# Kernel optimization log

Measured on AMD Instinct MI355X. Metric: run time of the kernel, lower is better.

## Reference

```python
import jax, jax.numpy as jnp
import numpy as np

N_NODES = 50000

def _graph_conv(x, src, dst, W, b, n):
    # DGL GraphConv, norm='both': D_dst^{-1/2} * sum_edges(D_src^{-1/2} * (x W)) + b
    xw = x @ W  # [N, out]
    ones = jnp.ones(src.shape, jnp.float32)
    deg_out = jnp.maximum(jax.ops.segment_sum(ones, src, num_segments=n), 1.0)
    deg_in = jnp.maximum(jax.ops.segment_sum(ones, dst, num_segments=n), 1.0)
    norm_src = deg_out ** -0.5
    norm_dst = deg_in ** -0.5
    msg = xw[src] * norm_src[src][:, None]          # [E, out] gather
    agg = jax.ops.segment_sum(msg, dst, num_segments=n)  # [N, out] scatter-add
    return agg * norm_dst[:, None] + b


def _rgcn_layer(x, src, dst, W, b, n):
    # HeteroGraphConv with aggregate='sum' over relations
    out = _graph_conv(x, src[0], dst[0], W[0], b[0], n)
    for r in range(1, src.shape[0]):
        out = out + _graph_conv(x, src[r], dst[r], W[r], b[r], n)
    return out


def setup_inputs() -> dict:
    key = jax.random.key(0)
    ks = jax.random.split(key, 9)
    R, E = 3, 200000
    din, dhid, dout = 128, 128, 64
    x = jax.random.normal(ks[0], (N_NODES, din), jnp.float32)
    src = jax.random.randint(ks[1], (R, E), 0, N_NODES, jnp.int32)
    dst = jax.random.randint(ks[2], (R, E), 0, N_NODES, jnp.int32)
    neg_src = jax.random.randint(ks[3], (E,), 0, N_NODES, jnp.int32)
    neg_dst = jax.random.randint(ks[4], (E,), 0, N_NODES, jnp.int32)
    W1 = jax.random.normal(ks[5], (R, din, dhid), jnp.float32) / np.sqrt(din)
    b1 = jnp.zeros((R, dhid), jnp.float32)
    W2 = jax.random.normal(ks[6], (R, dhid, dout), jnp.float32) / np.sqrt(dhid)
    b2 = jnp.zeros((R, dout), jnp.float32)
    return {"x": x, "src": src, "dst": dst, "neg_src": neg_src,
            "neg_dst": neg_dst, "W1": W1, "b1": b1, "W2": W2, "b2": b2}


def reference(x, src, dst, neg_src, neg_dst, W1, b1, W2, b2):
    n = x.shape[0]
    h = jax.nn.relu(_rgcn_layer(x, src, dst, W1, b1, n))
    h = _rgcn_layer(h, src, dst, W2, b2, n)  # [N, out]
    # HeteroDotProductPredictor on etype = relation 0 (u_dot_v -> [E, 1])
    pos = jnp.sum(h[src[0]] * h[dst[0]], axis=-1, keepdims=True)
    neg = jnp.sum(h[neg_src] * h[neg_dst], axis=-1, keepdims=True)
    return pos, neg
```

## Files before the change

kernel.cpp:

```cpp
#include <hip/hip_runtime.h>

#define N_NODES 50000
#define E_EDGES 200000
#define R_REL 3
#define D_IN 128
#define D_HID 128
#define D_OUT 64
#define N_SCAN (R_REL * N_NODES)
#define BCAP 16
#define OVCAP 4096

typedef __attribute__((ext_vector_type(8))) short bf16x8;
typedef __attribute__((ext_vector_type(4))) float f32x4;

__device__ inline unsigned short f2bf(float v) {
    union { float f; unsigned int u; } x; x.f = v;
    unsigned int r = x.u + 0x7fffu + ((x.u >> 16) & 1u);
    return (unsigned short)(r >> 16);
}
__device__ inline float bf2f(unsigned short h) {
    union { unsigned int u; float f; } x; x.u = ((unsigned int)h) << 16; return x.f;
}
__device__ inline float bf_lo(unsigned int p) {
    union { unsigned int u; float f; } x; x.u = p << 16; return x.f;
}
__device__ inline float bf_hi(unsigned int p) {
    union { unsigned int u; float f; } x; x.u = p & 0xffff0000u; return x.f;
}

__global__ __launch_bounds__(256) void k_zero_i32(int* __restrict__ p, int n) {
    int i = blockIdx.x * 256 + threadIdx.x;
    if (i < n) p[i] = 0;
}

__global__ __launch_bounds__(256) void k_count_prep(const int* __restrict__ src,
                                                    const int* __restrict__ dst,
                                                    const float* __restrict__ x,
                                                    const float* __restrict__ W1,
                                                    const float* __restrict__ W2,
                                                    const float* __restrict__ b1,
                                                    int* __restrict__ deg_out,
                                                    int* __restrict__ cnt_in,
                                                    int* __restrict__ ov_cnt,
                                                    uint2* __restrict__ ovlist,
                                                    int* __restrict__ bucket,
                                                    unsigned int* __restrict__ xb,
                                                    unsigned short* __restrict__ w1t_h,
                                                    unsigned short* __restrict__ w1t_l,
                                                    unsigned short* __restrict__ w2t_h,
                                                    unsigned short* __restrict__ w2t_l,
                                                    float* __restrict__ bsum) {
    int g = blockIdx.x / 5;
    int m = blockIdx.x % 5;
    int t = threadIdx.x;
    if (m < 3) {
        int eb = g * 3 + m;
        int i = eb * 256 + t;
        if (i >= R_REL * E_EDGES) return;
        int r = i / E_EDGES;
        int s = src[i];
        int d = dst[i];
        atomicAdd(&deg_out[r * N_NODES + s], 1);
        int bin = r * N_NODES + d;
        int pos = atomicAdd(&cnt_in[bin], 1);
        if (pos < BCAP) {
            bucket[bin * BCAP + pos] = s;
        } else {
            int oi = atomicAdd(ov_cnt, 1);
            if (oi < OVCAP) {
                uint2 e;
                e.x = (unsigned int)bin;
                e.y = (unsigned int)s;
                ovlist[oi] = e;
            }
        }
    } else {
        int pb = g * 2 + (m - 3);
        int qbase = pb * 1024;
#pragma unroll
        for (int k = 0; k < 4; k++) {
            int q = qbase + k * 256 + t;
            if (q < N_NODES * 32) {
                float4 v = ((const float4*)x)[q];
                uint2 u;
                u.x = ((unsigned int)f2bf(v.y) << 16) | f2bf(v.x);
                u.y = ((unsigned int)f2bf(v.w) << 16) | f2bf(v.z);
                ((uint2*)xb)[q] = u;
            }
        }
        int i = pb * 256 + t;
        if (i < R_REL * D_IN * D_HID) {
            int r = i >> 14;
            int kk = (i >> 7) & 127;
            int c = i & 127;
            float v = W1[i];
            unsigned short h = f2bf(v);
            unsigned short l = f2bf(v - bf2f(h));
            int o = r * 16384 + c * 128 + kk;
            w1t_h[o] = h;
            w1t_l[o] = l;
        }
        if (i < R_REL * D_HID * D_OUT) {
            int r = i >> 13;
            int kk = (i >> 6) & 127;
            int cl = i & 63;
            float v = W2[i];
            unsigned short h = f2bf(v);
            unsigned short l = f2bf(v - bf2f(h));
            int o = (r * 64 + cl) * 128 + kk;
            w2t_h[o] = h;
            w2t_l[o] = l;
        }
        if (i < 128) bsum[i] = b1[i] + b1[128 + i] + b1[256 + i];
    }
}

__global__ __launch_bounds__(256) void k_rednorm(const int* __restrict__ deg_out,
                                                 const int* __restrict__ cnt_in,
                                                 float* __restrict__ norm_out,
                                                 float* __restrict__ norm_in) {
    int b = blockIdx.x * 256 + threadIdx.x;
    if (b >= N_SCAN) return;
    int o = deg_out[b];
    int d = cnt_in[b];
    norm_out[b] = rsqrtf((float)(o > 1 ? o : 1));
    norm_in[b] = rsqrtf((float)(d > 1 ? d : 1));
}

__global__ __launch_bounds__(256) void k_aggall(const int* __restrict__ cnt_in,
                                                const int* __restrict__ bucket,
                                                const float* __restrict__ norm_out,
                                                const float* __restrict__ norm_in,
                                                const int* __restrict__ ov_cnt,
                                                const uint2* __restrict__ ovlist,
                                                const unsigned int* __restrict__ xb,
                                                unsigned int* __restrict__ aggh) {
    int w = (blockIdx.x * 256 + threadIdx.x) >> 6;
    if (w >= N_NODES) return;
    int lane = threadIdx.x & 63;
    const unsigned int* tab = xb + lane;
    int nn[R_REL];
    uint4 q[R_REL][4];
#pragma unroll
    for (int r = 0; r < R_REL; r++) {
        int bin = r * N_NODES + w;
        int n = cnt_in[bin];
        nn[r] = n < BCAP ? n : BCAP;
        const uint4* bp = (const uint4*)(bucket + bin * BCAP);
        q[r][0] = bp[0]; q[r][1] = bp[1]; q[r][2] = bp[2]; q[r][3] = bp[3];
    }
    int oc = *ov_cnt;
    if (oc > OVCAP) oc = OVCAP;
#pragma unroll
    for (int r = 0; r < R_REL; r++) {
        const float* nout = norm_out + r * N_NODES;
        unsigned int sl[BCAP] = {q[r][0].x, q[r][0].y, q[r][0].z, q[r][0].w,
                                 q[r][1].x, q[r][1].y, q[r][1].z, q[r][1].w,
                                 q[r][2].x, q[r][2].y, q[r][2].z, q[r][2].w,
                                 q[r][3].x, q[r][3].y, q[r][3].z, q[r][3].w};
        unsigned int p[BCAP];
        float c[BCAP];
#pragma unroll
        for (int j = 0; j < BCAP; j++) {
            if (j < nn[r]) {
                c[j] = nout[sl[j]];
                p[j] = tab[sl[j] * 64];
            }
        }
        float ax = 0.f, ay = 0.f;
#pragma unroll
        for (int j = 0; j < BCAP; j++) {
            if (j < nn[r]) {
                ax += c[j] * bf_lo(p[j]);
                ay += c[j] * bf_hi(p[j]);
            }
        }
        int bin = r * N_NODES + w;
        if (oc > 0) {
            for (int k = 0; k < oc; k++) {
                uint2 e = ovlist[k];
                if ((int)e.x == bin) {
                    float cc = nout[e.y];
                    unsigned int pp = tab[e.y * 64];
                    ax += cc * bf_lo(pp);
                    ay += cc * bf_hi(pp);
                }
            }
        }
        float ni = norm_in[bin];
        aggh[bin * 64 + lane] = ((unsigned int)f2bf(ay * ni) << 16) | f2bf(ax * ni);
    }
}

__global__ __launch_bounds__(256) void k_mm1f(const unsigned short* __restrict__ aggh,
                                              const unsigned short* __restrict__ wt_h,
                                              const unsigned short* __restrict__ wt_l,
                                              const float* __restrict__ bsum,
                                              unsigned short* __restrict__ h1h,
                                              unsigned short* __restrict__ h1l,
                                              int M) {
    __shared__ short sA[2048];
    __shared__ short sWh[4096], sWl[4096];
    int t = threadIdx.x;
    int row0 = blockIdx.x * 64;
    int wid = t >> 6;
    int lane = t & 63;
    int lr = lane & 15;
    int lkg = lane >> 4;
    int wr = (wid & 1) * 32;
    int wc = (wid >> 1) * 64;

    f32x4 acc[2][4];
#pragma unroll
    for (int i = 0; i < 2; i++)
#pragma unroll
        for (int j = 0; j < 4; j++) acc[i][j] = (f32x4)(0.f);

    int arow = t >> 2;
    int akg = t & 3;

    for (int k0 = 0; k0 < 384; k0 += 32) {
        int rr = k0 >> 7;
        int kk = k0 & 127;
        {
            int gr = row0 + arow;
            int cidx = akg * 64 + arow;
            if (gr < M)
                *(bf16x8*)&sA[cidx * 8] =
                    *(const bf16x8*)&aggh[(rr * N_NODES + gr) * 128 + kk + akg * 8];
            else
                *(bf16x8*)&sA[cidx * 8] = (bf16x8)(short)0;
        }
#pragma unroll
        for (int itr = 0; itr < 2; itr++) {
            int cc = t + itr * 256;
            int col = cc >> 2;
            int kg = cc & 3;
            int go = rr * 16384 + col * 128 + kk + kg * 8;
            int cidx = kg * 128 + col;
            *(bf16x8*)&sWh[cidx * 8] = *(const bf16x8*)&wt_h[go];
            *(bf16x8*)&sWl[cidx * 8] = *(const bf16x8*)&wt_l[go];
        }
        __syncthreads();
        bf16x8 a[2], bh[4], bl[4];
#pragma unroll
        for (int i = 0; i < 2; i++) {
            int cidx = lkg * 64 + wr + i * 16 + lr;
            a[i] = *(const bf16x8*)&sA[cidx * 8];
        }
#pragma unroll
        for (int j = 0; j < 4; j++) {
            int cidx = lkg * 128 + wc + j * 16 + lr;
            bh[j] = *(const bf16x8*)&sWh[cidx * 8];
            bl[j] = *(const bf16x8*)&sWl[cidx * 8];
        }
#pragma unroll
        for (int i = 0; i < 2; i++)
#pragma unroll
            for (int j = 0; j < 4; j++) {
                acc[i][j] = __builtin_amdgcn_mfma_f32_16x16x32_bf16(a[i], bh[j], acc[i][j], 0, 0, 0);
                acc[i][j] = __builtin_amdgcn_mfma_f32_16x16x32_bf16(a[i], bl[j], acc[i][j], 0, 0, 0);
            }
        __syncthreads();
    }
#pragma unroll
    for (int i = 0; i < 2; i++)
#pragma unroll
        for (int q = 0; q < 4; q++) {
            int gr = row0 + wr + i * 16 + lkg * 4 + q;
            if (gr >= M) continue;
#pragma unroll
            for (int j = 0; j < 4; j++) {
                int gc = wc + j * 16 + lr;
                float u = fmaxf(acc[i][j][q] + bsum[gc], 0.f);
                unsigned short h = f2bf(u);
                h1h[gr * 128 + gc] = h;
                h1l[gr * 128 + gc] = f2bf(u - bf2f(h));
            }
        }
}

__global__ __launch_bounds__(256) void k_mm2(const unsigned short* __restrict__ h1h,
                                             const unsigned short* __restrict__ h1l,
                                             const unsigned short* __restrict__ wt_h,
                                             const unsigned short* __restrict__ wt_l,
                                             const float* __restrict__ norm_out,
                                             unsigned short* __restrict__ xwb2, int M) {
    __shared__ short sAh[2048], sAl[2048];
    __shared__ short sWh[6144], sWl[6144];
    int t = threadIdx.x;
    int row0 = blockIdx.x * 64;
    int wid = t >> 6;
    int lane = t & 63;
    int lr = lane & 15;
    int lkg = lane >> 4;
    int wr = (wid & 1) * 32;
    int wc = (wid >> 1) * 96;

    f32x4 acc[2][6];
#pragma unroll
    for (int i = 0; i < 2; i++)
#pragma unroll
        for (int j = 0; j < 6; j++) acc[i][j] = (f32x4)(0.f);

    int arow = t >> 2;
    int akg = t & 3;

    for (int k0 = 0; k0 < 128; k0 += 32) {
        {
            int gr = row0 + arow;
            int cidx = akg * 64 + arow;
            if (gr < M) {
                int go = gr * 128 + k0 + akg * 8;
                *(bf16x8*)&sAh[cidx * 8] = *(const bf16x8*)&h1h[go];
                *(bf16x8*)&sAl[cidx * 8] = *(const bf16x8*)&h1l[go];
            } else {
                *(bf16x8*)&sAh[cidx * 8] = (bf16x8)(short)0;
                *(bf16x8*)&sAl[cidx * 8] = (bf16x8)(short)0;
            }
        }
#pragma unroll
        for (int itr = 0; itr < 3; itr++) {
            int cc = t + itr * 256;
            int col = cc >> 2;
            int kg = cc & 3;
            int go = col * 128 + k0 + kg * 8;
            int cidx = kg * 192 + col;
            *(bf16x8*)&sWh[cidx * 8] = *(const bf16x8*)&wt_h[go];
            *(bf16x8*)&sWl[cidx * 8] = *(const bf16x8*)&wt_l[go];
        }
        __syncthreads();
        bf16x8 ah[2], al[2];
#pragma unroll
        for (int i = 0; i < 2; i++) {
            int cidx = lkg * 64 + wr + i * 16 + lr;
            ah[i] = *(const bf16x8*)&sAh[cidx * 8];
            al[i] = *(const bf16x8*)&sAl[cidx * 8];
        }
#pragma unroll
        for (int j = 0; j < 6; j++) {
            int cidx = lkg * 192 + wc + j * 16 + lr;
            bf16x8 bh = *(const bf16x8*)&sWh[cidx * 8];
            bf16x8 bl = *(const bf16x8*)&sWl[cidx * 8];
#pragma unroll
            for (int i = 0; i < 2; i++) {
                acc[i][j] = __builtin_amdgcn_mfma_f32_16x16x32_bf16(ah[i], bh, acc[i][j], 0, 0, 0);
                acc[i][j] = __builtin_amdgcn_mfma_f32_16x16x32_bf16(ah[i], bl, acc[i][j], 0, 0, 0);
                acc[i][j] = __builtin_amdgcn_mfma_f32_16x16x32_bf16(al[i], bh, acc[i][j], 0, 0, 0);
            }
        }
        __syncthreads();
    }
#pragma unroll
    for (int i = 0; i < 2; i++)
#pragma unroll
        for (int q = 0; q < 4; q++) {
            int gr = row0 + wr + i * 16 + lkg * 4 + q;
            if (gr >= M) continue;
#pragma unroll
            for (int j = 0; j < 6; j++) {
                int gc = wc + j * 16 + lr;
                float sc = norm_out[(gc >> 6) * N_NODES + gr];
                xwb2[gr * 192 + gc] = f2bf(acc[i][j][q] * sc);
            }
        }
}

__global__ __launch_bounds__(256) void k_agg64f(const int* __restrict__ cnt_in,
                                                const int* __restrict__ bucket,
                                                const float* __restrict__ norm_in,
                                                const int* __restrict__ ov_cnt,
                                                const uint2* __restrict__ ovlist,
                                                const unsigned short* __restrict__ xwb,
                                                const float* __restrict__ b2,
                                                unsigned short* __restrict__ h2b) {
    int w = (blockIdx.x * 256 + threadIdx.x) >> 6;
    if (w >= N_NODES) return;
    int lane = threadIdx.x & 63;
    float acc = b2[lane] + b2[64 + lane] + b2[128 + lane];
    int oc = *ov_cnt;
    if (oc > OVCAP) oc = OVCAP;
#pragma unroll
    for (int r = 0; r < R_REL; r++) {
        const unsigned short* tab = xwb + r * 64 + lane;
        int bin = r * N_NODES + w;
        int n = cnt_in[bin];
        const uint4* bp = (const uint4*)(bucket + bin * BCAP);
        uint4 q0 = bp[0], q1 = bp[1], q2 = bp[2], q3 = bp[3];
        unsigned int sl[BCAP] = {q0.x, q0.y, q0.z, q0.w, q1.x, q1.y, q1.z, q1.w,
                                 q2.x, q2.y, q2.z, q2.w, q3.x, q3.y, q3.z, q3.w};
        int nn = n < BCAP ? n : BCAP;
        unsigned int pv[BCAP];
#pragma unroll
        for (int j = 0; j < BCAP; j++) {
            if (j < nn) pv[j] = tab[sl[j] * 192];
        }
        float a = 0.f;
#pragma unroll
        for (int j = 0; j < BCAP; j++) {
            if (j < nn) a += bf2f((unsigned short)pv[j]);
        }
        if (oc > 0) {
            for (int k = 0; k < oc; k++) {
                uint2 e = ovlist[k];
                if ((int)e.x == bin) a += bf2f(tab[e.y * 192]);
            }
        }
        acc += norm_in[bin] * a;
    }
    h2b[w * 64 + lane] = f2bf(acc);
}

__global__ __launch_bounds__(256) void k_predict(const int* __restrict__ sa,
                                                 const int* __restrict__ sb,
                                                 const int* __restrict__ na,
                                                 const int* __restrict__ nb,
                                                 const unsigned short* __restrict__ h2b,
                                                 float* __restrict__ out) {
    int tid = blockIdx.x * 256 + threadIdx.x;
    int p = tid >> 4;
    if (p >= 2 * E_EDGES) return;
    int lane = tid & 15;
    int ia, ib;
    if (p < E_EDGES) { ia = sa[p]; ib = sb[p]; }
    else             { ia = na[p - E_EDGES]; ib = nb[p - E_EDGES]; }
    uint2 ua = *(const uint2*)&h2b[ia * 64 + lane * 4];
    uint2 ub = *(const uint2*)&h2b[ib * 64 + lane * 4];
    float d = bf_lo(ua.x) * bf_lo(ub.x) + bf_hi(ua.x) * bf_hi(ub.x)
            + bf_lo(ua.y) * bf_lo(ub.y) + bf_hi(ua.y) * bf_hi(ub.y);
    d += __shfl_xor(d, 1);
    d += __shfl_xor(d, 2);
    d += __shfl_xor(d, 4);
    d += __shfl_xor(d, 8);
    if (lane == 0) out[p] = d;
}


extern "C" void kernel_launch(void* const* d_in, const int* in_sizes, int n_in,
                              void* d_out, int out_size, void* d_ws, size_t ws_size,
                              hipStream_t stream) {
    (void)in_sizes; (void)n_in; (void)out_size; (void)ws_size;
    const float* x       = (const float*)d_in[0];
    const int*   src     = (const int*)d_in[1];
    const int*   dst     = (const int*)d_in[2];
    const int*   neg_src = (const int*)d_in[3];
    const int*   neg_dst = (const int*)d_in[4];
    const float* W1      = (const float*)d_in[5];
    const float* b1      = (const float*)d_in[6];
    const float* W2      = (const float*)d_in[7];
    const float* b2      = (const float*)d_in[8];
    float* out = (float*)d_out;
    float* ws  = (float*)d_ws;

    float* norm_out = ws;
    float* norm_in  = ws + N_SCAN;
    int*   deg_out  = (int*)(ws + 300000);
    int*   cnt_in   = (int*)(ws + 450000);
    int*   ov_cnt   = (int*)(ws + 600000);
    uint2* ovlist   = (uint2*)(ws + 600016);
    int*   bucket   = (int*)(ws + 608208);
    unsigned short* w1t_h = (unsigned short*)(ws + 3008208);
    unsigned short* w1t_l = (unsigned short*)(ws + 3032784);
    unsigned short* w2t_h = (unsigned short*)(ws + 3057360);
    unsigned short* w2t_l = (unsigned short*)(ws + 3069648);
    float* bsum     = ws + 3081936;
    unsigned int*   aggh = (unsigned int*)(ws + 3082064);
    unsigned short* xwb2 = (unsigned short*)(ws + 3082064);
    unsigned short* h1h  = (unsigned short*)(ws + 12682064);
    unsigned short* h2b  = (unsigned short*)(ws + 12682064);
    unsigned short* h1l  = (unsigned short*)(ws + 15882064);
    unsigned int*   xb   = (unsigned int*)(ws + 15882064);

    const int NB_WAVE = (N_NODES * 64 + 255) / 256;
    const int NB_MM   = (N_NODES + 63) / 64;

    k_zero_i32<<<(300016 + 255) / 256, 256, 0, stream>>>(deg_out, 300016);
    k_count_prep<<<782 * 5, 256, 0, stream>>>(src, dst, x, W1, W2, b1,
                                              deg_out, cnt_in, ov_cnt, ovlist, bucket,
                                              xb, w1t_h, w1t_l, w2t_h, w2t_l, bsum);
    k_rednorm<<<(N_SCAN + 255) / 256, 256, 0, stream>>>(deg_out, cnt_in, norm_out, norm_in);

    k_aggall<<<NB_WAVE, 256, 0, stream>>>(cnt_in, bucket, norm_out, norm_in,
                                          ov_cnt, ovlist, xb, aggh);
    k_mm1f<<<NB_MM, 256, 0, stream>>>((const unsigned short*)aggh, w1t_h, w1t_l, bsum,
                                      h1h, h1l, N_NODES);

    k_mm2<<<NB_MM, 256, 0, stream>>>(h1h, h1l, w2t_h, w2t_l, norm_out, xwb2, N_NODES);
    k_agg64f<<<NB_WAVE, 256, 0, stream>>>(cnt_in, bucket, norm_in, ov_cnt, ovlist,
                                          xwb2, b2, h2b);

    k_predict<<<(2 * E_EDGES * 16 + 255) / 256, 256, 0, stream>>>(
        src, dst, neg_src, neg_dst, h2b, out);
}
```

Baseline: 250.3 us.

## Software-pipeline relation gathers in aggregation kernels and make xwb2 relation-major

Both aggregation kernels now issue the gathers for the next relation before consuming the current one, using double-buffered register arrays so more loads are in flight per wave. The layer-2 intermediate xwb2 moves from a [node][192] interleaved layout to three relation-major [relation][node][64] planes, so each gathered row is a contiguous 128-byte segment. The zeroing kernel is replaced with hipMemsetAsync. Keeping two stages of gathered values live raises register pressure, which may lower occupancy.

```diff
diff --git a/kernel.cpp b/kernel.cpp
--- a/kernel.cpp
+++ b/kernel.cpp
@@ -26,11 +26,6 @@
 }
 __device__ inline float bf_hi(unsigned int p) {
     union { unsigned int u; float f; } x; x.u = p & 0xffff0000u; return x.f;
-}
-
-__global__ __launch_bounds__(256) void k_zero_i32(int* __restrict__ p, int n) {
-    int i = blockIdx.x * 256 + threadIdx.x;
-    if (i < n) p[i] = 0;
 }
 
 __global__ __launch_bounds__(256) void k_count_prep(const int* __restrict__ src,
@@ -127,6 +122,12 @@
     norm_in[b] = rsqrtf((float)(d > 1 ? d : 1));
 }
 
+#define UNPK(dst, r) \
+    dst[0]=q[r][0].x; dst[1]=q[r][0].y; dst[2]=q[r][0].z; dst[3]=q[r][0].w; \
+    dst[4]=q[r][1].x; dst[5]=q[r][1].y; dst[6]=q[r][1].z; dst[7]=q[r][1].w; \
+    dst[8]=q[r][2].x; dst[9]=q[r][2].y; dst[10]=q[r][2].z; dst[11]=q[r][2].w; \
+    dst[12]=q[r][3].x; dst[13]=q[r][3].y; dst[14]=q[r][3].z; dst[15]=q[r][3].w;
+
 __global__ __launch_bounds__(256) void k_aggall(const int* __restrict__ cnt_in,
                                                 const int* __restrict__ bucket,
                                                 const float* __restrict__ norm_out,
@@ -151,45 +152,34 @@
     }
     int oc = *ov_cnt;
     if (oc > OVCAP) oc = OVCAP;
-#pragma unroll
-    for (int r = 0; r < R_REL; r++) {
-        const float* nout = norm_out + r * N_NODES;
-        unsigned int sl[BCAP] = {q[r][0].x, q[r][0].y, q[r][0].z, q[r][0].w,
-                                 q[r][1].x, q[r][1].y, q[r][1].z, q[r][1].w,
-                                 q[r][2].x, q[r][2].y, q[r][2].z, q[r][2].w,
-                                 q[r][3].x, q[r][3].y, q[r][3].z, q[r][3].w};
-        unsigned int p[BCAP];
-        float c[BCAP];
-#pragma unroll
-        for (int j = 0; j < BCAP; j++) {
-            if (j < nn[r]) {
-                c[j] = nout[sl[j]];
-                p[j] = tab[sl[j] * 64];
-            }
-        }
-        float ax = 0.f, ay = 0.f;
-#pragma unroll
-        for (int j = 0; j < BCAP; j++) {
-            if (j < nn[r]) {
-                ax += c[j] * bf_lo(p[j]);
-                ay += c[j] * bf_hi(p[j]);
-            }
-        }
-        int bin = r * N_NODES + w;
-        if (oc > 0) {
-            for (int k = 0; k < oc; k++) {
-                uint2 e = ovlist[k];
-                if ((int)e.x == bin) {
-                    float cc = nout[e.y];
-                    unsigned int pp = tab[e.y * 64];
-                    ax += cc * bf_lo(pp);
-                    ay += cc * bf_hi(pp);
-                }
-            }
-        }
-        float ni = norm_in[bin];
-        aggh[bin * 64 + lane] = ((unsigned int)f2bf(ay * ni) << 16) | f2bf(ax * ni);
-    }
+
+    unsigned int slA[BCAP], slB[BCAP];
+    unsigned int pA[BCAP], pB[BCAP];
+    float cA[BCAP], cB[BCAP];
+
+#define STAGE1(r, sl, cArr, pArr) { const float* nout = norm_out + (r) * N_NODES; \
+    _Pragma("unroll") \
+    for (int j = 0; j < BCAP; j++) if (j < nn[r]) { cArr[j] = nout[sl[j]]; pArr[j] = tab[sl[j] * 64]; } }
+
+#define CONSUME1(r, cArr, pArr) { float ax = 0.f, ay = 0.f; \
+    _Pragma("unroll") \
+    for (int j = 0; j < BCAP; j++) if (j < nn[r]) { ax += cArr[j] * bf_lo(pArr[j]); ay += cArr[j] * bf_hi(pArr[j]); } \
+    int bin = (r) * N_NODES + w; \
+    if (oc > 0) { const float* nout = norm_out + (r) * N_NODES; \
+        for (int k = 0; k < oc; k++) { uint2 e = ovlist[k]; \
+            if ((int)e.x == bin) { float cc = nout[e.y]; unsigned int pp = tab[e.y * 64]; \
+                ax += cc * bf_lo(pp); ay += cc * bf_hi(pp); } } } \
+    float ni = norm_in[bin]; \
+    aggh[bin * 64 + lane] = ((unsigned int)f2bf(ay * ni) << 16) | f2bf(ax * ni); }
+
+    UNPK(slA, 0); STAGE1(0, slA, cA, pA);
+    UNPK(slB, 1); STAGE1(1, slB, cB, pB);
+    CONSUME1(0, cA, pA);
+    UNPK(slA, 2); STAGE1(2, slA, cA, pA);
+    CONSUME1(1, cB, pB);
+    CONSUME1(2, cA, pA);
+#undef STAGE1
+#undef CONSUME1
 }
 
 __global__ __launch_bounds__(256) void k_mm1f(const unsigned short* __restrict__ aggh,
@@ -360,8 +350,10 @@
 #pragma unroll
             for (int j = 0; j < 6; j++) {
                 int gc = wc + j * 16 + lr;
-                float sc = norm_out[(gc >> 6) * N_NODES + gr];
-                xwb2[gr * 192 + gc] = f2bf(acc[i][j][q] * sc);
+                int rr = gc >> 6;
+                int cl = gc & 63;
+                float sc = norm_out[rr * N_NODES + gr];
+                xwb2[rr * (N_NODES * 64) + gr * 64 + cl] = f2bf(acc[i][j][q] * sc);
             }
         }
 }
@@ -380,34 +372,40 @@
     float acc = b2[lane] + b2[64 + lane] + b2[128 + lane];
     int oc = *ov_cnt;
     if (oc > OVCAP) oc = OVCAP;
+    int nn[R_REL];
+    uint4 q[R_REL][4];
 #pragma unroll
     for (int r = 0; r < R_REL; r++) {
-        const unsigned short* tab = xwb + r * 64 + lane;
         int bin = r * N_NODES + w;
         int n = cnt_in[bin];
+        nn[r] = n < BCAP ? n : BCAP;
         const uint4* bp = (const uint4*)(bucket + bin * BCAP);
-        uint4 q0 = bp[0], q1 = bp[1], q2 = bp[2], q3 = bp[3];
-        unsigned int sl[BCAP] = {q0.x, q0.y, q0.z, q0.w, q1.x, q1.y, q1.z, q1.w,
-                                 q2.x, q2.y, q2.z, q2.w, q3.x, q3.y, q3.z, q3.w};
-        int nn = n < BCAP ? n : BCAP;
-        unsigned int pv[BCAP];
-#pragma unroll
-        for (int j = 0; j < BCAP; j++) {
-            if (j < nn) pv[j] = tab[sl[j] * 192];
-        }
-        float a = 0.f;
-#pragma unroll
-        for (int j = 0; j < BCAP; j++) {
-            if (j < nn) a += bf2f((unsigned short)pv[j]);
-        }
-        if (oc > 0) {
-            for (int k = 0; k < oc; k++) {
-                uint2 e = ovlist[k];
-                if ((int)e.x == bin) a += bf2f(tab[e.y * 192]);
-            }
-        }
-        acc += norm_in[bin] * a;
+        q[r][0] = bp[0]; q[r][1] = bp[1]; q[r][2] = bp[2]; q[r][3] = bp[3];
     }
+    unsigned int slA[BCAP], slB[BCAP];
+    unsigned short pvA[BCAP], pvB[BCAP];
+
+#define STAGE2(r, sl, pv) { const unsigned short* tab = xwb + (r) * (N_NODES * 64) + lane; \
+    _Pragma("unroll") \
+    for (int j = 0; j < BCAP; j++) if (j < nn[r]) pv[j] = tab[sl[j] * 64]; }
+
+#define CONSUME2(r, pv) { float a = 0.f; \
+    _Pragma("unroll") \
+    for (int j = 0; j < BCAP; j++) if (j < nn[r]) a += bf2f(pv[j]); \
+    int bin = (r) * N_NODES + w; \
+    if (oc > 0) { const unsigned short* tab = xwb + (r) * (N_NODES * 64) + lane; \
+        for (int k = 0; k < oc; k++) { uint2 e = ovlist[k]; \
+            if ((int)e.x == bin) a += bf2f(tab[e.y * 64]); } } \
+    acc += norm_in[bin] * a; }
+
+    UNPK(slA, 0); STAGE2(0, slA, pvA);
+    UNPK(slB, 1); STAGE2(1, slB, pvB);
+    CONSUME2(0, pvA);
+    UNPK(slA, 2); STAGE2(2, slA, pvA);
+    CONSUME2(1, pvB);
+    CONSUME2(2, pvA);
+#undef STAGE2
+#undef CONSUME2
     h2b[w * 64 + lane] = f2bf(acc);
 }
 
@@ -474,7 +472,7 @@
     const int NB_WAVE = (N_NODES * 64 + 255) / 256;
     const int NB_MM   = (N_NODES + 63) / 64;
 
-    k_zero_i32<<<(300016 + 255) / 256, 256, 0, stream>>>(deg_out, 300016);
+    hipMemsetAsync(deg_out, 0, (size_t)300016 * sizeof(int), stream);
     k_count_prep<<<782 * 5, 256, 0, stream>>>(src, dst, x, W1, W2, b1,
                                               deg_out, cnt_in, ov_cnt, ovlist, bucket,
                                               xb, w1t_h, w1t_l, w2t_h, w2t_l, bsum);
```

Measured after the change: 279.9 us. +11.8%, slower.

## Fuse norm computation into aggregation and drop hidden-layer low-precision split

Applied to the files above, without the earlier changes.

Removes the separate norm kernel: the first aggregation computes the source and destination normalisation factors inline from the raw degree counts and also writes the norm arrays for later kernels. The layer-1 output is now stored only as a single bf16 array instead of a high/low split pair, which halves that write and read and removes one MFMA per step in the second matmul. The zeroing kernel becomes a hipMemsetAsync. The costs are extra rsqrt work per edge and lower precision in the hidden activations.

```diff
diff --git a/kernel.cpp b/kernel.cpp
--- a/kernel.cpp
+++ b/kernel.cpp
@@ -26,11 +26,6 @@
 }
 __device__ inline float bf_hi(unsigned int p) {
     union { unsigned int u; float f; } x; x.u = p & 0xffff0000u; return x.f;
-}
-
-__global__ __launch_bounds__(256) void k_zero_i32(int* __restrict__ p, int n) {
-    int i = blockIdx.x * 256 + threadIdx.x;
-    if (i < n) p[i] = 0;
 }
 
 __global__ __launch_bounds__(256) void k_count_prep(const int* __restrict__ src,
@@ -115,55 +110,56 @@
     }
 }
 
-__global__ __launch_bounds__(256) void k_rednorm(const int* __restrict__ deg_out,
-                                                 const int* __restrict__ cnt_in,
-                                                 float* __restrict__ norm_out,
-                                                 float* __restrict__ norm_in) {
-    int b = blockIdx.x * 256 + threadIdx.x;
-    if (b >= N_SCAN) return;
-    int o = deg_out[b];
-    int d = cnt_in[b];
-    norm_out[b] = rsqrtf((float)(o > 1 ? o : 1));
-    norm_in[b] = rsqrtf((float)(d > 1 ? d : 1));
-}
+#define UNPK(dst, r) \
+    dst[0]=q[r][0].x; dst[1]=q[r][0].y; dst[2]=q[r][0].z; dst[3]=q[r][0].w; \
+    dst[4]=q[r][1].x; dst[5]=q[r][1].y; dst[6]=q[r][1].z; dst[7]=q[r][1].w; \
+    dst[8]=q[r][2].x; dst[9]=q[r][2].y; dst[10]=q[r][2].z; dst[11]=q[r][2].w; \
+    dst[12]=q[r][3].x; dst[13]=q[r][3].y; dst[14]=q[r][3].z; dst[15]=q[r][3].w;
 
 __global__ __launch_bounds__(256) void k_aggall(const int* __restrict__ cnt_in,
                                                 const int* __restrict__ bucket,
-                                                const float* __restrict__ norm_out,
-                                                const float* __restrict__ norm_in,
+                                                const int* __restrict__ deg_out,
                                                 const int* __restrict__ ov_cnt,
                                                 const uint2* __restrict__ ovlist,
                                                 const unsigned int* __restrict__ xb,
-                                                unsigned int* __restrict__ aggh) {
+                                                unsigned int* __restrict__ aggh,
+                                                float* __restrict__ norm_out,
+                                                float* __restrict__ norm_in) {
     int w = (blockIdx.x * 256 + threadIdx.x) >> 6;
     if (w >= N_NODES) return;
     int lane = threadIdx.x & 63;
     const unsigned int* tab = xb + lane;
-    int nn[R_REL];
+    int nn[R_REL], nraw[R_REL];
     uint4 q[R_REL][4];
 #pragma unroll
     for (int r = 0; r < R_REL; r++) {
         int bin = r * N_NODES + w;
         int n = cnt_in[bin];
+        nraw[r] = n;
         nn[r] = n < BCAP ? n : BCAP;
         const uint4* bp = (const uint4*)(bucket + bin * BCAP);
         q[r][0] = bp[0]; q[r][1] = bp[1]; q[r][2] = bp[2]; q[r][3] = bp[3];
     }
+    if (lane < R_REL) {
+        int bin = lane * N_NODES + w;
+        int nr = lane == 0 ? nraw[0] : (lane == 1 ? nraw[1] : nraw[2]);
+        norm_in[bin] = rsqrtf((float)(nr > 1 ? nr : 1));
+        int dd = deg_out[bin];
+        norm_out[bin] = rsqrtf((float)(dd > 1 ? dd : 1));
+    }
     int oc = *ov_cnt;
     if (oc > OVCAP) oc = OVCAP;
 #pragma unroll
     for (int r = 0; r < R_REL; r++) {
-        const float* nout = norm_out + r * N_NODES;
-        unsigned int sl[BCAP] = {q[r][0].x, q[r][0].y, q[r][0].z, q[r][0].w,
-                                 q[r][1].x, q[r][1].y, q[r][1].z, q[r][1].w,
-                                 q[r][2].x, q[r][2].y, q[r][2].z, q[r][2].w,
-                                 q[r][3].x, q[r][3].y, q[r][3].z, q[r][3].w};
+        const int* dout = deg_out + r * N_NODES;
+        unsigned int sl[BCAP];
+        UNPK(sl, r);
+        int dg[BCAP];
         unsigned int p[BCAP];
-        float c[BCAP];
 #pragma unroll
         for (int j = 0; j < BCAP; j++) {
             if (j < nn[r]) {
-                c[j] = nout[sl[j]];
+                dg[j] = dout[sl[j]];
                 p[j] = tab[sl[j] * 64];
             }
         }
@@ -171,8 +167,9 @@
 #pragma unroll
         for (int j = 0; j < BCAP; j++) {
             if (j < nn[r]) {
-                ax += c[j] * bf_lo(p[j]);
-                ay += c[j] * bf_hi(p[j]);
+                float c = rsqrtf((float)(dg[j] > 1 ? dg[j] : 1));
+                ax += c * bf_lo(p[j]);
+                ay += c * bf_hi(p[j]);
             }
         }
         int bin = r * N_NODES + w;
@@ -180,14 +177,15 @@
             for (int k = 0; k < oc; k++) {
                 uint2 e = ovlist[k];
                 if ((int)e.x == bin) {
-                    float cc = nout[e.y];
+                    int dd = dout[e.y];
+                    float cc = rsqrtf((float)(dd > 1 ? dd : 1));
                     unsigned int pp = tab[e.y * 64];
                     ax += cc * bf_lo(pp);
                     ay += cc * bf_hi(pp);
                 }
             }
         }
-        float ni = norm_in[bin];
+        float ni = rsqrtf((float)(nraw[r] > 1 ? nraw[r] : 1));
         aggh[bin * 64 + lane] = ((unsigned int)f2bf(ay * ni) << 16) | f2bf(ax * ni);
     }
 }
@@ -197,7 +195,6 @@
                                               const unsigned short* __restrict__ wt_l,
                                               const float* __restrict__ bsum,
                                               unsigned short* __restrict__ h1h,
-                                              unsigned short* __restrict__ h1l,
                                               int M) {
     __shared__ short sA[2048];
     __shared__ short sWh[4096], sWl[4096];
@@ -273,20 +270,17 @@
             for (int j = 0; j < 4; j++) {
                 int gc = wc + j * 16 + lr;
                 float u = fmaxf(acc[i][j][q] + bsum[gc], 0.f);
-                unsigned short h = f2bf(u);
-                h1h[gr * 128 + gc] = h;
-                h1l[gr * 128 + gc] = f2bf(u - bf2f(h));
+                h1h[gr * 128 + gc] = f2bf(u);
             }
         }
 }
 
 __global__ __launch_bounds__(256) void k_mm2(const unsigned short* __restrict__ h1h,
-                                             const unsigned short* __restrict__ h1l,
                                              const unsigned short* __restrict__ wt_h,
                                              const unsigned short* __restrict__ wt_l,
                                              const float* __restrict__ norm_out,
                                              unsigned short* __restrict__ xwb2, int M) {
-    __shared__ short sAh[2048], sAl[2048];
+    __shared__ short sA[2048];
     __shared__ short sWh[6144], sWl[6144];
     int t = threadIdx.x;
     int row0 = blockIdx.x * 64;
@@ -310,14 +304,10 @@
         {
             int gr = row0 + arow;
             int cidx = akg * 64 + arow;
-            if (gr < M) {
-                int go = gr * 128 + k0 + akg * 8;
-                *(bf16x8*)&sAh[cidx * 8] = *(const bf16x8*)&h1h[go];
-                *(bf16x8*)&sAl[cidx * 8] = *(const bf16x8*)&h1l[go];
-            } else {
-                *(bf16x8*)&sAh[cidx * 8] = (bf16x8)(short)0;
-                *(bf16x8*)&sAl[cidx * 8] = (bf16x8)(short)0;
-            }
+            if (gr < M)
+                *(bf16x8*)&sA[cidx * 8] = *(const bf16x8*)&h1h[gr * 128 + k0 + akg * 8];
+            else
+                *(bf16x8*)&sA[cidx * 8] = (bf16x8)(short)0;
         }
 #pragma unroll
         for (int itr = 0; itr < 3; itr++) {
@@ -330,12 +320,11 @@
             *(bf16x8*)&sWl[cidx * 8] = *(const bf16x8*)&wt_l[go];
         }
         __syncthreads();
-        bf16x8 ah[2], al[2];
+        bf16x8 a[2];
 #pragma unroll
         for (int i = 0; i < 2; i++) {
             int cidx = lkg * 64 + wr + i * 16 + lr;
-            ah[i] = *(const bf16x8*)&sAh[cidx * 8];
-            al[i] = *(const bf16x8*)&sAl[cidx * 8];
+            a[i] = *(const bf16x8*)&sA[cidx * 8];
         }
 #pragma unroll
         for (int j = 0; j < 6; j++) {
@@ -344,9 +333,8 @@
             bf16x8 bl = *(const bf16x8*)&sWl[cidx * 8];
 #pragma unroll
             for (int i = 0; i < 2; i++) {
-                acc[i][j] = __builtin_amdgcn_mfma_f32_16x16x32_bf16(ah[i], bh, acc[i][j], 0, 0, 0);
-                acc[i][j] = __builtin_amdgcn_mfma_f32_16x16x32_bf16(ah[i], bl, acc[i][j], 0, 0, 0);
-                acc[i][j] = __builtin_amdgcn_mfma_f32_16x16x32_bf16(al[i], bh, acc[i][j], 0, 0, 0);
+                acc[i][j] = __builtin_amdgcn_mfma_f32_16x16x32_bf16(a[i], bh, acc[i][j], 0, 0, 0);
+                acc[i][j] = __builtin_amdgcn_mfma_f32_16x16x32_bf16(a[i], bl, acc[i][j], 0, 0, 0);
             }
         }
         __syncthreads();
@@ -390,7 +378,7 @@
         unsigned int sl[BCAP] = {q0.x, q0.y, q0.z, q0.w, q1.x, q1.y, q1.z, q1.w,
                                  q2.x, q2.y, q2.z, q2.w, q3.x, q3.y, q3.z, q3.w};
         int nn = n < BCAP ? n : BCAP;
-        unsigned int pv[BCAP];
+        unsigned short pv[BCAP];
 #pragma unroll
         for (int j = 0; j < BCAP; j++) {
             if (j < nn) pv[j] = tab[sl[j] * 192];
@@ -398,7 +386,7 @@
         float a = 0.f;
 #pragma unroll
         for (int j = 0; j < BCAP; j++) {
-            if (j < nn) a += bf2f((unsigned short)pv[j]);
+            if (j < nn) a += bf2f(pv[j]);
         }
         if (oc > 0) {
             for (int k = 0; k < oc; k++) {
@@ -468,24 +456,22 @@
     unsigned short* xwb2 = (unsigned short*)(ws + 3082064);
     unsigned short* h1h  = (unsigned short*)(ws + 12682064);
     unsigned short* h2b  = (unsigned short*)(ws + 12682064);
-    unsigned short* h1l  = (unsigned short*)(ws + 15882064);
     unsigned int*   xb   = (unsigned int*)(ws + 15882064);
 
     const int NB_WAVE = (N_NODES * 64 + 255) / 256;
     const int NB_MM   = (N_NODES + 63) / 64;
 
-    k_zero_i32<<<(300016 + 255) / 256, 256, 0, stream>>>(deg_out, 300016);
+    hipMemsetAsync(deg_out, 0, (size_t)300016 * sizeof(int), stream);
     k_count_prep<<<782 * 5, 256, 0, stream>>>(src, dst, x, W1, W2, b1,
                                               deg_out, cnt_in, ov_cnt, ovlist, bucket,
                                               xb, w1t_h, w1t_l, w2t_h, w2t_l, bsum);
-    k_rednorm<<<(N_SCAN + 255) / 256, 256, 0, stream>>>(deg_out, cnt_in, norm_out, norm_in);
-
-    k_aggall<<<NB_WAVE, 256, 0, stream>>>(cnt_in, bucket, norm_out, norm_in,
-                                          ov_cnt, ovlist, xb, aggh);
+
+    k_aggall<<<NB_WAVE, 256, 0, stream>>>(cnt_in, bucket, deg_out, ov_cnt, ovlist,
+                                          xb, aggh, norm_out, norm_in);
     k_mm1f<<<NB_MM, 256, 0, stream>>>((const unsigned short*)aggh, w1t_h, w1t_l, bsum,
-                                      h1h, h1l, N_NODES);
-
-    k_mm2<<<NB_MM, 256, 0, stream>>>(h1h, h1l, w2t_h, w2t_l, norm_out, xwb2, N_NODES);
+                                      h1h, N_NODES);
+
+    k_mm2<<<NB_MM, 256, 0, stream>>>(h1h, w2t_h, w2t_l, norm_out, xwb2, N_NODES);
     k_agg64f<<<NB_WAVE, 256, 0, stream>>>(cnt_in, bucket, norm_in, ov_cnt, ovlist,
                                           xwb2, b2, h2b);
 
```

Measured after the change: 251.1 us. No clear change (+0.3%).
